# Performance work log

Measured on AMD Instinct MI355X. Metric: run time of the kernel, lower is better.

The kernel has to match this reference:

```python
import jax, jax.numpy as jnp
import numpy as np

B, P, C = 256, 256, 512
EPS = 1e-6

def setup_inputs() -> dict:
    key = jax.random.key(0)
    ks = jax.random.split(key, 9)
    s_p = 1.0 / np.sqrt(P)
    s_c = 1.0 / np.sqrt(C)
    return {
        "x": jax.random.normal(ks[0], (B, P, C), dtype=jnp.float32),
        "ln_g": jnp.ones((C,), jnp.float32),
        "ln_b": jnp.zeros((C,), jnp.float32),
        # token-mixing MLP (P -> P -> P)
        "w1a": jax.random.normal(ks[1], (P, P), jnp.float32) * s_p,
        "b1a": jnp.zeros((P,), jnp.float32),
        "w1b": jax.random.normal(ks[2], (P, P), jnp.float32) * s_p,
        "b1b": jnp.zeros((P,), jnp.float32),
        # channel-mixing MLP (C -> C -> C)
        "w2a": jax.random.normal(ks[3], (C, C), jnp.float32) * s_c,
        "b2a": jnp.zeros((C,), jnp.float32),
        "w2b": jax.random.normal(ks[4], (C, C), jnp.float32) * s_c,
        "b2b": jnp.zeros((C,), jnp.float32),
    }

def _layernorm(v, g, b):
    mu = jnp.mean(v, axis=-1, keepdims=True)
    var = jnp.mean(jnp.square(v - mu), axis=-1, keepdims=True)
    return (v - mu) * jax.lax.rsqrt(var + EPS) * g + b

def reference(x, ln_g, ln_b, w1a, b1a, w1b, b1b, w2a, b2a, w2b, b2b):
    # token mixing: normalize, transpose to [B, C, P], MLP over P, transpose back
    h = _layernorm(x, ln_g, ln_b)                       # [B, P, C]
    ht = jnp.swapaxes(h, 1, 2)                          # [B, C, P]
    t = jax.nn.gelu(ht @ w1a + b1a, approximate=False) @ w1b + b1b
    x = jnp.swapaxes(t, 1, 2) + x                       # residual with original input
    # channel mixing: note residual adds to the NORMALIZED x (as in source)
    h = _layernorm(x, ln_g, ln_b)                       # [B, P, C]
    t2 = jax.nn.gelu(h @ w2a + b2a, approximate=False) @ w2b + b2b
    return h + t2
```

## Files before the change

kernel.cpp:

```cpp
#include <hip/hip_runtime.h>
#include <hip/hip_bf16.h>
#include <math.h>

typedef __bf16 bf16x8 __attribute__((ext_vector_type(8)));
typedef float f32x4 __attribute__((ext_vector_type(4)));
typedef unsigned short u16x8 __attribute__((ext_vector_type(8)));

#define DEV __device__ __forceinline__

DEV unsigned short f2bf(float f){ __hip_bfloat16 h=__float2bfloat16(f); unsigned short u; __builtin_memcpy(&u,&h,2); return u; }
DEV float bf2f(unsigned short u){ __hip_bfloat16 h; __builtin_memcpy(&h,&u,2); return __bfloat162float(h); }

DEV float gelu_f(float v){
  float u = v*(0.7978845608f + 0.0356774081f*v*v);
  float e = __expf(2.0f*u);
  float t = 1.0f - 2.0f*__builtin_amdgcn_rcpf(e + 1.0f);
  return 0.5f*v*(1.0f + t);
}

DEV void gl2lds16(const void* g, void* l){
  __builtin_amdgcn_global_load_lds((const __attribute__((address_space(1))) void*)g,
                                   (__attribute__((address_space(3))) void*)l, 16, 0, 0);
}

__global__ __launch_bounds__(256) void k_wt(const float* __restrict__ W,
                                            unsigned short* __restrict__ WT,
                                            int K, int N){
  int i = blockIdx.x*256 + threadIdx.x;
  if (i >= K*N) return;
  int k = i % K, n = i / K;
  WT[i] = f2bf(W[(size_t)k*N + n]);
}

__global__ __launch_bounds__(256) void k_ln1x(const float* __restrict__ x,
                                              const float* __restrict__ g,
                                              const float* __restrict__ be,
                                              unsigned short* __restrict__ ht,
                                              unsigned short* __restrict__ xb){
  __shared__ unsigned short tile[32][512];
  int blk = blockIdx.x;
  int b = blk >> 3, p0 = (blk & 7) << 5;
  int tid = threadIdx.x, w = tid >> 6, l = tid & 63;
  float4 gv0 = *(const float4*)(g  + l*8);
  float4 gv1 = *(const float4*)(g  + l*8 + 4);
  float4 bv0 = *(const float4*)(be + l*8);
  float4 bv1 = *(const float4*)(be + l*8 + 4);
  const float* xbase = x + (((size_t)b << 8) + p0) * 512;
  for (int i = 0; i < 8; ++i) {
    int pl = (i << 2) + w;
    const float* row = xbase + (size_t)pl*512 + l*8;
    float4 v0 = *(const float4*)row;
    float4 v1 = *(const float4*)(row + 4);
    u16x8 rc;
    rc[0]=f2bf(v0.x); rc[1]=f2bf(v0.y); rc[2]=f2bf(v0.z); rc[3]=f2bf(v0.w);
    rc[4]=f2bf(v1.x); rc[5]=f2bf(v1.y); rc[6]=f2bf(v1.z); rc[7]=f2bf(v1.w);
    *(u16x8*)(xb + (((size_t)b << 8) + p0 + pl)*512 + l*8) = rc;
    float s  = v0.x+v0.y+v0.z+v0.w + v1.x+v1.y+v1.z+v1.w;
    float s2 = v0.x*v0.x+v0.y*v0.y+v0.z*v0.z+v0.w*v0.w
             + v1.x*v1.x+v1.y*v1.y+v1.z*v1.z+v1.w*v1.w;
    #pragma unroll
    for (int off = 32; off; off >>= 1){ s += __shfl_xor(s, off); s2 += __shfl_xor(s2, off); }
    float mu = s * (1.0f/512.0f);
    float rs = rsqrtf(s2*(1.0f/512.0f) - mu*mu + 1e-6f);
    u16x8 o;
    o[0]=f2bf((v0.x-mu)*rs*gv0.x+bv0.x);
    o[1]=f2bf((v0.y-mu)*rs*gv0.y+bv0.y);
    o[2]=f2bf((v0.z-mu)*rs*gv0.z+bv0.z);
    o[3]=f2bf((v0.w-mu)*rs*gv0.w+bv0.w);
    o[4]=f2bf((v1.x-mu)*rs*gv1.x+bv1.x);
    o[5]=f2bf((v1.y-mu)*rs*gv1.y+bv1.y);
    o[6]=f2bf((v1.z-mu)*rs*gv1.z+bv1.z);
    o[7]=f2bf((v1.w-mu)*rs*gv1.w+bv1.w);
    *(u16x8*)(&tile[pl][l*8]) = o;
  }
  __syncthreads();
  unsigned short* hb = ht + ((size_t)b << 17);
  #pragma unroll
  for (int it = 0; it < 8; ++it) {
    int c = (it << 6) + (tid >> 2);
    int pch = (tid & 3) << 3;
    u16x8 o;
    #pragma unroll
    for (int j = 0; j < 8; ++j) o[j] = tile[pch + j][c];
    *(u16x8*)(hb + (size_t)c*256 + p0 + pch) = o;
  }
}

__global__ __launch_bounds__(256) void k_tl2(const unsigned short* __restrict__ t,
                                             const unsigned short* __restrict__ xb,
                                             const float* __restrict__ g,
                                             const float* __restrict__ be,
                                             unsigned short* __restrict__ h2){
  __shared__ unsigned short th[32][520];
  int blk = blockIdx.x;
  int b = blk >> 3, p0 = (blk & 7) << 5;
  int tid = threadIdx.x, w = tid >> 6, l = tid & 63;
  const unsigned short* tb = t + ((size_t)b << 17) + p0;
  #pragma unroll
  for (int it = 0; it < 8; ++it){
    int fc = (it << 8) + tid;
    int c = fc >> 2, pch = (fc & 3) << 3;
    u16x8 tv = *(const u16x8*)(tb + (size_t)c*256 + pch);
    #pragma unroll
    for (int j = 0; j < 8; ++j) th[pch + j][c] = tv[j];
  }
  __syncthreads();
  float4 gv0 = *(const float4*)(g  + l*8);
  float4 gv1 = *(const float4*)(g  + l*8 + 4);
  float4 bv0 = *(const float4*)(be + l*8);
  float4 bv1 = *(const float4*)(be + l*8 + 4);
  #pragma unroll
  for (int it = 0; it < 8; ++it){
    int pl = (it << 2) + w;
    u16x8 tvv = *(const u16x8*)(&th[pl][l*8]);
    size_t rowo = (((size_t)b << 8) + p0 + pl)*512 + l*8;
    u16x8 xvv = *(const u16x8*)(xb + rowo);
    float v[8];
    #pragma unroll
    for (int j = 0; j < 8; ++j) v[j] = bf2f(tvv[j]) + bf2f(xvv[j]);
    float s = 0.f, s2 = 0.f;
    #pragma unroll
    for (int j = 0; j < 8; ++j){ s += v[j]; s2 += v[j]*v[j]; }
    #pragma unroll
    for (int off = 32; off; off >>= 1){ s += __shfl_xor(s, off); s2 += __shfl_xor(s2, off); }
    float mu = s * (1.0f/512.0f);
    float rs = rsqrtf(s2*(1.0f/512.0f) - mu*mu + 1e-6f);
    u16x8 o;
    o[0]=f2bf((v[0]-mu)*rs*gv0.x+bv0.x);
    o[1]=f2bf((v[1]-mu)*rs*gv0.y+bv0.y);
    o[2]=f2bf((v[2]-mu)*rs*gv0.z+bv0.z);
    o[3]=f2bf((v[3]-mu)*rs*gv0.w+bv0.w);
    o[4]=f2bf((v[4]-mu)*rs*gv1.x+bv1.x);
    o[5]=f2bf((v[5]-mu)*rs*gv1.y+bv1.y);
    o[6]=f2bf((v[6]-mu)*rs*gv1.z+bv1.z);
    o[7]=f2bf((v[7]-mu)*rs*gv1.w+bv1.w);
    *(u16x8*)(h2 + rowo) = o;
  }
}

template<int R>
DEV void stageTile(const unsigned short* src, int rowStride, char* ldst, int tid){
  #pragma unroll
  for (int i = 0; i < (R*8)/512; ++i){
    int q = (i << 9) + tid;
    int row = q >> 3, sc = q & 7;
    int cc = sc ^ (row & 7);
    gl2lds16(src + (size_t)row*rowStride + (cc << 3), ldst + q*16);
  }
}

template<int MT, int NT, int MODE>
__global__ __launch_bounds__(512, 2) void k_mlp(
    const unsigned short* __restrict__ A,
    const unsigned short* __restrict__ W1T,
    const unsigned short* __restrict__ W2T,
    const float* __restrict__ b1v,
    const float* __restrict__ b2v,
    unsigned short* __restrict__ outb,
    float* __restrict__ outf)
{
  constexpr int WN = NT/64;
  constexpr int KT = NT/64;
  constexpr int CHR = NT/8;
  __shared__ char lds[MT*128 + NT*128 + MT*NT*2];
  char* lsA = lds;
  char* lsW = lds + MT*128;
  char* U   = lds + MT*128 + NT*128;
  const int tid = threadIdx.x;
  const int w = tid >> 6, l = tid & 63;
  const int wm = w / WN, wn = w % WN;
  const int la = l & 15, lg = l >> 4;
  const size_t m0 = (size_t)blockIdx.x * MT;
  const unsigned short* Ab = A + m0*NT;

  f32x4 acc[4][4];
  #pragma unroll
  for (int i = 0; i < 4; ++i)
    #pragma unroll
    for (int j = 0; j < 4; ++j) acc[i][j] = (f32x4){0.f,0.f,0.f,0.f};

  for (int kt = 0; kt < KT; ++kt){
    stageTile<MT>(Ab  + (kt << 6), NT, lsA, tid);
    stageTile<NT>(W1T + (kt << 6), NT, lsW, tid);
    __syncthreads();
    #pragma unroll
    for (int ks = 0; ks < 2; ++ks){
      bf16x8 af[4], bfr[4];
      int c = (ks << 2) + lg;
      #pragma unroll
      for (int mi = 0; mi < 4; ++mi){
        int rr = (wm << 6) + (mi << 4) + la;
        af[mi] = *(const bf16x8*)(lsA + rr*128 + ((c ^ (rr & 7)) << 4));
      }
      #pragma unroll
      for (int ni = 0; ni < 4; ++ni){
        int rn = (wn << 6) + (ni << 4) + la;
        bfr[ni] = *(const bf16x8*)(lsW + rn*128 + ((c ^ (rn & 7)) << 4));
      }
      #pragma unroll
      for (int mi = 0; mi < 4; ++mi)
        #pragma unroll
        for (int ni = 0; ni < 4; ++ni)
          acc[mi][ni] = __builtin_amdgcn_mfma_f32_16x16x32_bf16(af[mi], bfr[ni], acc[mi][ni], 0, 0, 0);
    }
    __syncthreads();
  }
  #pragma unroll
  for (int ni = 0; ni < 4; ++ni){
    int col = (wn << 6) + (ni << 4) + la;
    float bv = b1v[col];
    #pragma unroll
    for (int mi = 0; mi < 4; ++mi){
      int rb = (wm << 6) + (mi << 4) + (lg << 2);
      #pragma unroll
      for (int rg = 0; rg < 4; ++rg){
        float v = gelu_f(acc[mi][ni][rg] + bv);
        int r = rb + rg;
        *(unsigned short*)(U + ((size_t)r*NT + ((((col >> 3) ^ (r & 7)) << 3) + (col & 7)))*2) = f2bf(v);
        acc[mi][ni][rg] = 0.0f;
      }
    }
  }
  __syncthreads();
  for (int kt = 0; kt < KT; ++kt){
    stageTile<NT>(W2T + (kt << 6), NT, lsW, tid);
    __syncthreads();
    #pragma unroll
    for (int ks = 0; ks < 2; ++ks){
      bf16x8 af[4], bfr[4];
      int c = (ks << 2) + lg;
      int cki = (kt << 3) + c;
      #pragma unroll
      for (int mi = 0; mi < 4; ++mi){
        int rr = (wm << 6) + (mi << 4) + la;
        af[mi] = *(const bf16x8*)(U + (size_t)rr*NT*2 + ((cki ^ (rr & 7)) << 4));
      }
      #pragma unroll
      for (int ni = 0; ni < 4; ++ni){
        int rn = (wn << 6) + (ni << 4) + la;
        bfr[ni] = *(const bf16x8*)(lsW + rn*128 + ((c ^ (rn & 7)) << 4));
      }
      #pragma unroll
      for (int mi = 0; mi < 4; ++mi)
        #pragma unroll
        for (int ni = 0; ni < 4; ++ni)
          acc[mi][ni] = __builtin_amdgcn_mfma_f32_16x16x32_bf16(af[mi], bfr[ni], acc[mi][ni], 0, 0, 0);
    }
    __syncthreads();
  }
  #pragma unroll
  for (int ni = 0; ni < 4; ++ni){
    int col = (wn << 6) + (ni << 4) + la;
    float bv = b2v[col];
    #pragma unroll
    for (int mi = 0; mi < 4; ++mi){
      int rb = (wm << 6) + (mi << 4) + (lg << 2);
      #pragma unroll
      for (int rg = 0; rg < 4; ++rg){
        float v = acc[mi][ni][rg] + bv;
        int r = rb + rg;
        *(unsigned short*)(U + ((size_t)r*NT + ((((col >> 3) ^ (r & 7)) << 3) + (col & 7)))*2) = f2bf(v);
      }
    }
  }
  __syncthreads();
  #pragma unroll
  for (int i = 0; i < (MT*CHR)/512; ++i){
    int q = (i << 9) + tid;
    int r = q / CHR, ck = q % CHR;
    u16x8 val = *(const u16x8*)(U + (size_t)r*NT*2 + ((ck ^ (r & 7)) << 4));
    size_t go = (m0 + r)*NT + (ck << 3);
    if (MODE == 0){
      *(u16x8*)(outb + go) = val;
    } else {
      u16x8 av = *(const u16x8*)(Ab + (size_t)r*NT + (ck << 3));
      float4 o0, o1;
      o0.x = bf2f(val[0]) + bf2f(av[0]);
      o0.y = bf2f(val[1]) + bf2f(av[1]);
      o0.z = bf2f(val[2]) + bf2f(av[2]);
      o0.w = bf2f(val[3]) + bf2f(av[3]);
      o1.x = bf2f(val[4]) + bf2f(av[4]);
      o1.y = bf2f(val[5]) + bf2f(av[5]);
      o1.z = bf2f(val[6]) + bf2f(av[6]);
      o1.w = bf2f(val[7]) + bf2f(av[7]);
      *(float4*)(outf + go)     = o0;
      *(float4*)(outf + go + 4) = o1;
    }
  }
}

extern "C" void kernel_launch(void* const* d_in, const int* in_sizes, int n_in,
                              void* d_out, int out_size, void* d_ws, size_t ws_size,
                              hipStream_t stream) {
  const float* x   = (const float*)d_in[0];
  const float* lng = (const float*)d_in[1];
  const float* lnb = (const float*)d_in[2];
  const float* w1a = (const float*)d_in[3];
  const float* b1a = (const float*)d_in[4];
  const float* w1b = (const float*)d_in[5];
  const float* b1b = (const float*)d_in[6];
  const float* w2a = (const float*)d_in[7];
  const float* b2a = (const float*)d_in[8];
  const float* w2b = (const float*)d_in[9];
  const float* b2b = (const float*)d_in[10];
  float* out = (float*)d_out;
  char* ws = (char*)d_ws;
  unsigned short* bufA = (unsigned short*)ws;
  unsigned short* bufB = (unsigned short*)(ws + (size_t)(64u << 20));
  unsigned short* wt1a = (unsigned short*)(ws + (size_t)(128u << 20));
  unsigned short* wt1b = wt1a + 256*256;
  unsigned short* wt2a = wt1b + 256*256;
  unsigned short* wt2b = wt2a + 512*512;
  unsigned short* xb   = (unsigned short*)d_out;

  k_wt<<<256,  256, 0, stream>>>(w1a, wt1a, 256, 256);
  k_wt<<<256,  256, 0, stream>>>(w1b, wt1b, 256, 256);
  k_wt<<<1024, 256, 0, stream>>>(w2a, wt2a, 512, 512);
  k_wt<<<1024, 256, 0, stream>>>(w2b, wt2b, 512, 512);

  k_ln1x<<<2048, 256, 0, stream>>>(x, lng, lnb, bufA, xb);
  k_mlp<128, 256, 0><<<1024, 512, 0, stream>>>(bufA, wt1a, wt1b, b1a, b1b, bufB, nullptr);

  k_tl2<<<2048, 256, 0, stream>>>(bufB, xb, lng, lnb, bufA);

  k_mlp<64, 512, 1><<<1024, 512, 0, stream>>>(bufA, wt2a, wt2b, b2a, b2b, nullptr, out);
}
```

Before: 322.5 us.

## Restructure fused MLP kernel to small row tiles with weights read from global

The fused two-layer MLP kernel now processes 32-row tiles with one wave per 64 output columns. Weight fragments are loaded directly from global memory (relying on L2/cache) instead of being staged through LDS each k-step, and the whole A tile is staged into LDS once up front. This removes the per-k-tile barriers and doubles or quadruples the grid size with higher occupancy bounds. The trade-off is less reuse of each weight load across rows and more redundant weight traffic from global/L2. The residual in the second MLP is also read from the LDS-resident A tile instead of from global.

```diff
diff --git a/kernel.cpp b/kernel.cpp
--- a/kernel.cpp
+++ b/kernel.cpp
@@ -138,19 +138,8 @@
   }
 }
 
-template<int R>
-DEV void stageTile(const unsigned short* src, int rowStride, char* ldst, int tid){
-  #pragma unroll
-  for (int i = 0; i < (R*8)/512; ++i){
-    int q = (i << 9) + tid;
-    int row = q >> 3, sc = q & 7;
-    int cc = sc ^ (row & 7);
-    gl2lds16(src + (size_t)row*rowStride + (cc << 3), ldst + q*16);
-  }
-}
-
-template<int MT, int NT, int MODE>
-__global__ __launch_bounds__(512, 2) void k_mlp(
+template<int MT, int K, int NT, int MODE>
+__global__ __launch_bounds__(NT, 4) void k_mlp(
     const unsigned short* __restrict__ A,
     const unsigned short* __restrict__ W1T,
     const unsigned short* __restrict__ W2T,
@@ -159,121 +148,121 @@
     unsigned short* __restrict__ outb,
     float* __restrict__ outf)
 {
-  constexpr int WN = NT/64;
-  constexpr int KT = NT/64;
-  constexpr int CHR = NT/8;
-  __shared__ char lds[MT*128 + NT*128 + MT*NT*2];
-  char* lsA = lds;
-  char* lsW = lds + MT*128;
-  char* U   = lds + MT*128 + NT*128;
+  constexpr int CHA = K/8;
+  constexpr int CHU = NT/8;
+  constexpr int MI  = MT/16;
+  __shared__ char lsA[MT*K*2];
+  __shared__ char U[MT*NT*2];
   const int tid = threadIdx.x;
-  const int w = tid >> 6, l = tid & 63;
-  const int wm = w / WN, wn = w % WN;
+  const int wn = tid >> 6, l = tid & 63;
   const int la = l & 15, lg = l >> 4;
   const size_t m0 = (size_t)blockIdx.x * MT;
-  const unsigned short* Ab = A + m0*NT;
-
-  f32x4 acc[4][4];
-  #pragma unroll
-  for (int i = 0; i < 4; ++i)
+  const unsigned short* Ab = A + m0*K;
+
+  #pragma unroll
+  for (int i = 0; i < (MT*CHA)/NT; ++i){
+    int q = i*NT + tid;
+    int row = q / CHA, sc = q % CHA;
+    int cc = sc ^ (row & 7);
+    gl2lds16(Ab + (size_t)row*K + (cc << 3), lsA + q*16);
+  }
+  f32x4 acc[MI][4];
+  #pragma unroll
+  for (int i = 0; i < MI; ++i)
     #pragma unroll
     for (int j = 0; j < 4; ++j) acc[i][j] = (f32x4){0.f,0.f,0.f,0.f};
-
-  for (int kt = 0; kt < KT; ++kt){
-    stageTile<MT>(Ab  + (kt << 6), NT, lsA, tid);
-    stageTile<NT>(W1T + (kt << 6), NT, lsW, tid);
-    __syncthreads();
-    #pragma unroll
-    for (int ks = 0; ks < 2; ++ks){
-      bf16x8 af[4], bfr[4];
-      int c = (ks << 2) + lg;
+  __syncthreads();
+
+  #pragma unroll
+  for (int ks = 0; ks < K/32; ++ks){
+    int c = (ks << 2) + lg;
+    bf16x8 af[MI], bfr[4];
+    #pragma unroll
+    for (int mi = 0; mi < MI; ++mi){
+      int rr = (mi << 4) + la;
+      af[mi] = *(const bf16x8*)(lsA + ((size_t)rr*CHA + (c ^ (rr & 7)))*16);
+    }
+    #pragma unroll
+    for (int ni = 0; ni < 4; ++ni){
+      int rn = (wn << 6) + (ni << 4) + la;
+      bfr[ni] = *(const bf16x8*)(W1T + (size_t)rn*K + (c << 3));
+    }
+    #pragma unroll
+    for (int mi = 0; mi < MI; ++mi)
       #pragma unroll
-      for (int mi = 0; mi < 4; ++mi){
-        int rr = (wm << 6) + (mi << 4) + la;
-        af[mi] = *(const bf16x8*)(lsA + rr*128 + ((c ^ (rr & 7)) << 4));
-      }
-      #pragma unroll
-      for (int ni = 0; ni < 4; ++ni){
-        int rn = (wn << 6) + (ni << 4) + la;
-        bfr[ni] = *(const bf16x8*)(lsW + rn*128 + ((c ^ (rn & 7)) << 4));
-      }
-      #pragma unroll
-      for (int mi = 0; mi < 4; ++mi)
-        #pragma unroll
-        for (int ni = 0; ni < 4; ++ni)
-          acc[mi][ni] = __builtin_amdgcn_mfma_f32_16x16x32_bf16(af[mi], bfr[ni], acc[mi][ni], 0, 0, 0);
-    }
-    __syncthreads();
-  }
+      for (int ni = 0; ni < 4; ++ni)
+        acc[mi][ni] = __builtin_amdgcn_mfma_f32_16x16x32_bf16(af[mi], bfr[ni], acc[mi][ni], 0, 0, 0);
+  }
+
   #pragma unroll
   for (int ni = 0; ni < 4; ++ni){
     int col = (wn << 6) + (ni << 4) + la;
     float bv = b1v[col];
-    #pragma unroll
-    for (int mi = 0; mi < 4; ++mi){
-      int rb = (wm << 6) + (mi << 4) + (lg << 2);
+    int ck = col >> 3, cw = col & 7;
+    #pragma unroll
+    for (int mi = 0; mi < MI; ++mi){
+      int rb = (mi << 4) + (lg << 2);
       #pragma unroll
       for (int rg = 0; rg < 4; ++rg){
         float v = gelu_f(acc[mi][ni][rg] + bv);
         int r = rb + rg;
-        *(unsigned short*)(U + ((size_t)r*NT + ((((col >> 3) ^ (r & 7)) << 3) + (col & 7)))*2) = f2bf(v);
+        *(unsigned short*)(U + ((size_t)r*NT + (((ck ^ (r & 7)) << 3) + cw))*2) = f2bf(v);
         acc[mi][ni][rg] = 0.0f;
       }
     }
   }
   __syncthreads();
-  for (int kt = 0; kt < KT; ++kt){
-    stageTile<NT>(W2T + (kt << 6), NT, lsW, tid);
-    __syncthreads();
-    #pragma unroll
-    for (int ks = 0; ks < 2; ++ks){
-      bf16x8 af[4], bfr[4];
-      int c = (ks << 2) + lg;
-      int cki = (kt << 3) + c;
+
+  #pragma unroll
+  for (int ks = 0; ks < NT/32; ++ks){
+    int c = (ks << 2) + lg;
+    bf16x8 af[MI], bfr[4];
+    #pragma unroll
+    for (int mi = 0; mi < MI; ++mi){
+      int rr = (mi << 4) + la;
+      af[mi] = *(const bf16x8*)(U + ((size_t)rr*CHU + (c ^ (rr & 7)))*16);
+    }
+    #pragma unroll
+    for (int ni = 0; ni < 4; ++ni){
+      int rn = (wn << 6) + (ni << 4) + la;
+      bfr[ni] = *(const bf16x8*)(W2T + (size_t)rn*NT + (c << 3));
+    }
+    #pragma unroll
+    for (int mi = 0; mi < MI; ++mi)
       #pragma unroll
-      for (int mi = 0; mi < 4; ++mi){
-        int rr = (wm << 6) + (mi << 4) + la;
-        af[mi] = *(const bf16x8*)(U + (size_t)rr*NT*2 + ((cki ^ (rr & 7)) << 4));
-      }
-      #pragma unroll
-      for (int ni = 0; ni < 4; ++ni){
-        int rn = (wn << 6) + (ni << 4) + la;
-        bfr[ni] = *(const bf16x8*)(lsW + rn*128 + ((c ^ (rn & 7)) << 4));
-      }
-      #pragma unroll
-      for (int mi = 0; mi < 4; ++mi)
-        #pragma unroll
-        for (int ni = 0; ni < 4; ++ni)
-          acc[mi][ni] = __builtin_amdgcn_mfma_f32_16x16x32_bf16(af[mi], bfr[ni], acc[mi][ni], 0, 0, 0);
-    }
-    __syncthreads();
-  }
+      for (int ni = 0; ni < 4; ++ni)
+        acc[mi][ni] = __builtin_amdgcn_mfma_f32_16x16x32_bf16(af[mi], bfr[ni], acc[mi][ni], 0, 0, 0);
+  }
+  __syncthreads();
+
   #pragma unroll
   for (int ni = 0; ni < 4; ++ni){
     int col = (wn << 6) + (ni << 4) + la;
     float bv = b2v[col];
-    #pragma unroll
-    for (int mi = 0; mi < 4; ++mi){
-      int rb = (wm << 6) + (mi << 4) + (lg << 2);
+    int ck = col >> 3, cw = col & 7;
+    #pragma unroll
+    for (int mi = 0; mi < MI; ++mi){
+      int rb = (mi << 4) + (lg << 2);
       #pragma unroll
       for (int rg = 0; rg < 4; ++rg){
         float v = acc[mi][ni][rg] + bv;
         int r = rb + rg;
-        *(unsigned short*)(U + ((size_t)r*NT + ((((col >> 3) ^ (r & 7)) << 3) + (col & 7)))*2) = f2bf(v);
+        *(unsigned short*)(U + ((size_t)r*NT + (((ck ^ (r & 7)) << 3) + cw))*2) = f2bf(v);
       }
     }
   }
   __syncthreads();
-  #pragma unroll
-  for (int i = 0; i < (MT*CHR)/512; ++i){
-    int q = (i << 9) + tid;
-    int r = q / CHR, ck = q % CHR;
-    u16x8 val = *(const u16x8*)(U + (size_t)r*NT*2 + ((ck ^ (r & 7)) << 4));
+
+  #pragma unroll
+  for (int i = 0; i < (MT*CHU)/NT; ++i){
+    int q = i*NT + tid;
+    int r = q / CHU, ck = q % CHU;
+    u16x8 val = *(const u16x8*)(U + ((size_t)r*CHU + (ck ^ (r & 7)))*16);
     size_t go = (m0 + r)*NT + (ck << 3);
     if (MODE == 0){
       *(u16x8*)(outb + go) = val;
     } else {
-      u16x8 av = *(const u16x8*)(Ab + (size_t)r*NT + (ck << 3));
+      u16x8 av = *(const u16x8*)(lsA + ((size_t)r*CHA + (ck ^ (r & 7)))*16);
       float4 o0, o1;
       o0.x = bf2f(val[0]) + bf2f(av[0]);
       o0.y = bf2f(val[1]) + bf2f(av[1]);
@@ -319,9 +308,9 @@
   k_wt<<<1024, 256, 0, stream>>>(w2b, wt2b, 512, 512);
 
   k_ln1x<<<2048, 256, 0, stream>>>(x, lng, lnb, bufA, xb);
-  k_mlp<128, 256, 0><<<1024, 512, 0, stream>>>(bufA, wt1a, wt1b, b1a, b1b, bufB, nullptr);
+  k_mlp<32, 256, 256, 0><<<4096, 256, 0, stream>>>(bufA, wt1a, wt1b, b1a, b1b, bufB, nullptr);
 
   k_tl2<<<2048, 256, 0, stream>>>(bufB, xb, lng, lnb, bufA);
 
-  k_mlp<64, 512, 1><<<1024, 512, 0, stream>>>(bufA, wt2a, wt2b, b2a, b2b, nullptr, out);
-}
+  k_mlp<32, 512, 512, 1><<<2048, 512, 0, stream>>>(bufA, wt2a, wt2b, b2a, b2b, nullptr, out);
+}
```

After: 504.9 us. 1.57x slower.

## Split fused two-layer MLP kernels into separate tiled GEMM kernels

Applied to the files above, without the earlier changes.

Replaces the fused MLP kernel, which kept the full hidden activation in LDS, with a generic 128x128-tiled GEMM kernel launched twice per MLP, with the intermediate written to global memory in bf16. It adds an XCD-aware block remap and a per-wave padded LDS epilogue for coalesced stores. The aim is smaller LDS use, higher occupancy and more blocks to spread across CUs. The cost is extra global round-trips for the hidden activations and two more kernel launches.

```diff
diff --git a/kernel.cpp b/kernel.cpp
--- a/kernel.cpp
+++ b/kernel.cpp
@@ -138,40 +138,33 @@
   }
 }
 
-template<int R>
-DEV void stageTile(const unsigned short* src, int rowStride, char* ldst, int tid){
-  #pragma unroll
-  for (int i = 0; i < (R*8)/512; ++i){
-    int q = (i << 9) + tid;
-    int row = q >> 3, sc = q & 7;
-    int cc = sc ^ (row & 7);
-    gl2lds16(src + (size_t)row*rowStride + (cc << 3), ldst + q*16);
-  }
-}
-
-template<int MT, int NT, int MODE>
-__global__ __launch_bounds__(512, 2) void k_mlp(
+template<int N, int KT, int MODE>
+__global__ __launch_bounds__(256, 2) void k_gemm(
     const unsigned short* __restrict__ A,
-    const unsigned short* __restrict__ W1T,
-    const unsigned short* __restrict__ W2T,
-    const float* __restrict__ b1v,
-    const float* __restrict__ b2v,
+    const unsigned short* __restrict__ BT,
+    const float* __restrict__ bias,
     unsigned short* __restrict__ outb,
-    float* __restrict__ outf)
+    float* __restrict__ outf,
+    const unsigned short* __restrict__ res)
 {
-  constexpr int WN = NT/64;
-  constexpr int KT = NT/64;
-  constexpr int CHR = NT/8;
-  __shared__ char lds[MT*128 + NT*128 + MT*NT*2];
+  constexpr int K = KT*64;
+  constexpr int nTn = N/128;
+  constexpr int EPITCH = 176;
+  constexpr int EREG   = 64*EPITCH;
+  __shared__ char lds[4*EREG];
   char* lsA = lds;
-  char* lsW = lds + MT*128;
-  char* U   = lds + MT*128 + NT*128;
+  char* lsB = lds + 16384;
+
+  int nwg = gridDim.x, bid = blockIdx.x;
+  int wgid = ((nwg & 7) == 0) ? ((bid & 7)*(nwg >> 3) + (bid >> 3)) : bid;
+  int tm = wgid / nTn, tn = wgid % nTn;
+  size_t m0 = (size_t)tm * 128;
+  int n0 = tn * 128;
+
   const int tid = threadIdx.x;
   const int w = tid >> 6, l = tid & 63;
-  const int wm = w / WN, wn = w % WN;
+  const int wm = w >> 1, wn = w & 1;
   const int la = l & 15, lg = l >> 4;
-  const size_t m0 = (size_t)blockIdx.x * MT;
-  const unsigned short* Ab = A + m0*NT;
 
   f32x4 acc[4][4];
   #pragma unroll
@@ -180,22 +173,29 @@
     for (int j = 0; j < 4; ++j) acc[i][j] = (f32x4){0.f,0.f,0.f,0.f};
 
   for (int kt = 0; kt < KT; ++kt){
-    stageTile<MT>(Ab  + (kt << 6), NT, lsA, tid);
-    stageTile<NT>(W1T + (kt << 6), NT, lsW, tid);
+    int kb = kt << 6;
+    #pragma unroll
+    for (int i = 0; i < 4; ++i){
+      int q = (i << 8) + tid;
+      int row = q >> 3, sc = q & 7;
+      int cc = sc ^ (row & 7);
+      gl2lds16(A  + (m0 + row)*K + kb + (cc << 3), lsA + q*16);
+      gl2lds16(BT + (size_t)(n0 + row)*K + kb + (cc << 3), lsB + q*16);
+    }
     __syncthreads();
     #pragma unroll
     for (int ks = 0; ks < 2; ++ks){
+      int c = (ks << 2) + lg;
       bf16x8 af[4], bfr[4];
-      int c = (ks << 2) + lg;
       #pragma unroll
       for (int mi = 0; mi < 4; ++mi){
         int rr = (wm << 6) + (mi << 4) + la;
-        af[mi] = *(const bf16x8*)(lsA + rr*128 + ((c ^ (rr & 7)) << 4));
+        af[mi] = *(const bf16x8*)(lsA + ((rr << 3) + (c ^ (rr & 7)))*16);
       }
       #pragma unroll
       for (int ni = 0; ni < 4; ++ni){
         int rn = (wn << 6) + (ni << 4) + la;
-        bfr[ni] = *(const bf16x8*)(lsW + rn*128 + ((c ^ (rn & 7)) << 4));
+        bfr[ni] = *(const bf16x8*)(lsB + ((rn << 3) + (c ^ (rn & 7)))*16);
       }
       #pragma unroll
       for (int mi = 0; mi < 4; ++mi)
@@ -205,84 +205,45 @@
     }
     __syncthreads();
   }
+
+  char* ep = lds + w*EREG;
   #pragma unroll
   for (int ni = 0; ni < 4; ++ni){
-    int col = (wn << 6) + (ni << 4) + la;
-    float bv = b1v[col];
+    int colw = (ni << 4) + la;
+    float bv = bias[n0 + (wn << 6) + colw];
     #pragma unroll
     for (int mi = 0; mi < 4; ++mi){
-      int rb = (wm << 6) + (mi << 4) + (lg << 2);
-      #pragma unroll
-      for (int rg = 0; rg < 4; ++rg){
-        float v = gelu_f(acc[mi][ni][rg] + bv);
-        int r = rb + rg;
-        *(unsigned short*)(U + ((size_t)r*NT + ((((col >> 3) ^ (r & 7)) << 3) + (col & 7)))*2) = f2bf(v);
-        acc[mi][ni][rg] = 0.0f;
-      }
-    }
-  }
-  __syncthreads();
-  for (int kt = 0; kt < KT; ++kt){
-    stageTile<NT>(W2T + (kt << 6), NT, lsW, tid);
-    __syncthreads();
-    #pragma unroll
-    for (int ks = 0; ks < 2; ++ks){
-      bf16x8 af[4], bfr[4];
-      int c = (ks << 2) + lg;
-      int cki = (kt << 3) + c;
-      #pragma unroll
-      for (int mi = 0; mi < 4; ++mi){
-        int rr = (wm << 6) + (mi << 4) + la;
-        af[mi] = *(const bf16x8*)(U + (size_t)rr*NT*2 + ((cki ^ (rr & 7)) << 4));
-      }
-      #pragma unroll
-      for (int ni = 0; ni < 4; ++ni){
-        int rn = (wn << 6) + (ni << 4) + la;
-        bfr[ni] = *(const bf16x8*)(lsW + rn*128 + ((c ^ (rn & 7)) << 4));
-      }
-      #pragma unroll
-      for (int mi = 0; mi < 4; ++mi)
-        #pragma unroll
-        for (int ni = 0; ni < 4; ++ni)
-          acc[mi][ni] = __builtin_amdgcn_mfma_f32_16x16x32_bf16(af[mi], bfr[ni], acc[mi][ni], 0, 0, 0);
-    }
-    __syncthreads();
-  }
-  #pragma unroll
-  for (int ni = 0; ni < 4; ++ni){
-    int col = (wn << 6) + (ni << 4) + la;
-    float bv = b2v[col];
-    #pragma unroll
-    for (int mi = 0; mi < 4; ++mi){
-      int rb = (wm << 6) + (mi << 4) + (lg << 2);
       #pragma unroll
       for (int rg = 0; rg < 4; ++rg){
         float v = acc[mi][ni][rg] + bv;
-        int r = rb + rg;
-        *(unsigned short*)(U + ((size_t)r*NT + ((((col >> 3) ^ (r & 7)) << 3) + (col & 7)))*2) = f2bf(v);
+        if (MODE == 0) v = gelu_f(v);
+        int r = (mi << 4) + (lg << 2) + rg;
+        *(unsigned short*)(ep + r*EPITCH + colw*2) = f2bf(v);
       }
     }
   }
   __syncthreads();
-  #pragma unroll
-  for (int i = 0; i < (MT*CHR)/512; ++i){
-    int q = (i << 9) + tid;
-    int r = q / CHR, ck = q % CHR;
-    u16x8 val = *(const u16x8*)(U + (size_t)r*NT*2 + ((ck ^ (r & 7)) << 4));
-    size_t go = (m0 + r)*NT + (ck << 3);
-    if (MODE == 0){
+
+  #pragma unroll
+  for (int i = 0; i < 8; ++i){
+    int q = (i << 8) + tid;
+    int r = q >> 4, ck = q & 15;
+    int wreg = ((r >> 6) << 1) | (ck >> 3);
+    u16x8 val = *(const u16x8*)(lds + wreg*EREG + (r & 63)*EPITCH + (ck & 7)*16);
+    size_t go = (m0 + r)*N + n0 + (ck << 3);
+    if (MODE != 2){
       *(u16x8*)(outb + go) = val;
     } else {
-      u16x8 av = *(const u16x8*)(Ab + (size_t)r*NT + (ck << 3));
+      u16x8 rv = *(const u16x8*)(res + go);
       float4 o0, o1;
-      o0.x = bf2f(val[0]) + bf2f(av[0]);
-      o0.y = bf2f(val[1]) + bf2f(av[1]);
-      o0.z = bf2f(val[2]) + bf2f(av[2]);
-      o0.w = bf2f(val[3]) + bf2f(av[3]);
-      o1.x = bf2f(val[4]) + bf2f(av[4]);
-      o1.y = bf2f(val[5]) + bf2f(av[5]);
-      o1.z = bf2f(val[6]) + bf2f(av[6]);
-      o1.w = bf2f(val[7]) + bf2f(av[7]);
+      o0.x = bf2f(val[0]) + bf2f(rv[0]);
+      o0.y = bf2f(val[1]) + bf2f(rv[1]);
+      o0.z = bf2f(val[2]) + bf2f(rv[2]);
+      o0.w = bf2f(val[3]) + bf2f(rv[3]);
+      o1.x = bf2f(val[4]) + bf2f(rv[4]);
+      o1.y = bf2f(val[5]) + bf2f(rv[5]);
+      o1.z = bf2f(val[6]) + bf2f(rv[6]);
+      o1.w = bf2f(val[7]) + bf2f(rv[7]);
       *(float4*)(outf + go)     = o0;
       *(float4*)(outf + go + 4) = o1;
     }
@@ -319,9 +280,11 @@
   k_wt<<<1024, 256, 0, stream>>>(w2b, wt2b, 512, 512);
 
   k_ln1x<<<2048, 256, 0, stream>>>(x, lng, lnb, bufA, xb);
-  k_mlp<128, 256, 0><<<1024, 512, 0, stream>>>(bufA, wt1a, wt1b, b1a, b1b, bufB, nullptr);
-
-  k_tl2<<<2048, 256, 0, stream>>>(bufB, xb, lng, lnb, bufA);
-
-  k_mlp<64, 512, 1><<<1024, 512, 0, stream>>>(bufA, wt2a, wt2b, b2a, b2b, nullptr, out);
-}
+  k_gemm<256, 4, 0><<<2048, 256, 0, stream>>>(bufA, wt1a, b1a, bufB, nullptr, nullptr);
+  k_gemm<256, 4, 1><<<2048, 256, 0, stream>>>(bufB, wt1b, b1b, bufA, nullptr, nullptr);
+
+  k_tl2<<<2048, 256, 0, stream>>>(bufA, xb, lng, lnb, bufB);
+
+  k_gemm<512, 8, 0><<<2048, 256, 0, stream>>>(bufB, wt2a, b2a, bufA, nullptr, nullptr);
+  k_gemm<512, 8, 2><<<2048, 256, 0, stream>>>(bufA, wt2b, b2b, nullptr, out, bufB);
+}
```

Result: faster. 293.2 us (-9.1%).
